# Optimization experiments

Hardware: AMD Instinct MI355X
Metric: run time of the kernel (lower is better)

Reference implementation:

```python
import jax, jax.numpy as jnp
import numpy as np

B, N, FEAT = 64, 1024, 3
HID, STATE, LAYERS, NTYPES = 64, 32, 2, 10


def setup_inputs() -> dict:
    key = jax.random.key(0)
    ks = jax.random.split(key, 16)
    s = 0.1
    return {
        "task_features": jax.random.normal(ks[0], (B, N, FEAT), jnp.float32),
        "task_types": jax.random.randint(ks[1], (B, N), 0, NTYPES, jnp.int32),
        "prev_state": jnp.zeros((B, STATE), jnp.float32),
        "enc_w1": jax.random.normal(ks[2], (HID, FEAT), jnp.float32) * s,
        "enc_b1": jnp.zeros((HID,), jnp.float32),
        "enc_w2": jax.random.normal(ks[3], (HID, HID), jnp.float32) * s,
        "enc_b2": jnp.zeros((HID,), jnp.float32),
        "contention": jax.random.normal(ks[4], (NTYPES, NTYPES), jnp.float32) * 0.1,
        "gnn_w": jax.random.normal(ks[5], (LAYERS, HID, HID), jnp.float32) * s,
        "gnn_b": jnp.zeros((LAYERS, HID), jnp.float32),
        "gru_w_ih": jax.random.normal(ks[6], (3 * STATE, HID), jnp.float32) * s,
        "gru_w_hh": jax.random.normal(ks[7], (3 * STATE, STATE), jnp.float32) * s,
        "gru_b_ih": jnp.zeros((3 * STATE,), jnp.float32),
        "gru_b_hh": jnp.zeros((3 * STATE,), jnp.float32),
        "head_w1": jax.random.normal(ks[8], (HID, HID + STATE), jnp.float32) * s,
        "head_b1": jnp.zeros((HID,), jnp.float32),
        "head_w2": jax.random.normal(ks[9], (1, HID), jnp.float32) * s,
        "head_b2": jnp.zeros((1,), jnp.float32),
    }


def _forward(task_features, task_types, prev_state, enc_w1, enc_b1, enc_w2, enc_b2,
             contention, gnn_w, gnn_b, gru_w_ih, gru_w_hh, gru_b_ih, gru_b_hh,
             head_w1, head_b1, head_w2, head_b2):
    # task encoder: Linear -> ReLU -> Linear
    emb = jax.nn.relu(task_features @ enc_w1.T + enc_b1) @ enc_w2.T + enc_b2  # (B,N,H)
    # interaction graph: type-pair gather + cosine similarity
    base = contention[task_types[:, :, None], task_types[:, None, :]]  # (B,N,N)
    nrm = emb / jnp.maximum(jnp.linalg.norm(emb, axis=-1, keepdims=True), 1e-12)
    sim = jnp.einsum("bnd,bmd->bnm", nrm, nrm)
    adjacency = jax.nn.sigmoid(base) * sim  # (B,N,N)
    # GNN layers: aggregate + linear + relu
    h = emb
    for l in range(LAYERS):
        agg = jnp.einsum("bnm,bmd->bnd", adjacency, h)
        h = jax.nn.relu((h + agg) @ gnn_w[l].T + gnn_b[l])
    ctx = h.mean(axis=1)  # (B,H)
    # GRUCell (torch semantics)
    gi = ctx @ gru_w_ih.T + gru_b_ih
    gh = prev_state @ gru_w_hh.T + gru_b_hh
    i_r, i_z, i_n = jnp.split(gi, 3, axis=-1)
    h_r, h_z, h_n = jnp.split(gh, 3, axis=-1)
    r = jax.nn.sigmoid(i_r + h_r)
    z = jax.nn.sigmoid(i_z + h_z)
    n = jnp.tanh(i_n + r * h_n)
    new_state = (1.0 - z) * n + z * prev_state  # (B,S)
    # latency head on [h, state]
    st = jnp.broadcast_to(new_state[:, None, :], (h.shape[0], h.shape[1], new_state.shape[-1]))
    combined = jnp.concatenate([h, st], axis=-1)
    lat = jax.nn.relu(combined @ head_w1.T + head_b1) @ head_w2.T + head_b2
    return lat[..., 0], new_state


def reference(task_features, task_types, prev_state, enc_w1, enc_b1, enc_w2, enc_b2,
              contention, gnn_w, gnn_b, gru_w_ih, gru_w_hh, gru_b_ih, gru_b_hh,
              head_w1, head_b1, head_w2, head_b2):
    return _forward(task_features, task_types, prev_state, enc_w1, enc_b1, enc_w2, enc_b2,
                    contention, gnn_w, gnn_b, gru_w_ih, gru_w_hh, gru_b_ih, gru_b_hh,
                    head_w1, head_b1, head_w2, head_b2)
```

## Files before the change

kernel.cpp:

```cpp
#include <hip/hip_runtime.h>
#include <math.h>

#define BB 64
#define NN 1024
#define HID 64
#define STATE 32
#define NTYPES 10

typedef _Float16 f16;
typedef f16 f16x8 __attribute__((ext_vector_type(8)));
typedef f16 f16x4 __attribute__((ext_vector_type(4)));
typedef float f32x4 __attribute__((ext_vector_type(4)));

#define MFMA16(a, b, c) __builtin_amdgcn_mfma_f32_16x16x32_f16(a, b, c, 0, 0, 0)

__device__ __forceinline__ float sigm(float x) { return 1.f / (1.f + expf(-x)); }

__device__ __forceinline__ f16x8 cvt8(float4 a, float4 b) {
    f16x8 r;
    r[0] = (f16)a.x; r[1] = (f16)a.y; r[2] = (f16)a.z; r[3] = (f16)a.w;
    r[4] = (f16)b.x; r[5] = (f16)b.y; r[6] = (f16)b.z; r[7] = (f16)b.w;
    return r;
}
__device__ __forceinline__ unsigned packh2(f16 a, f16 b) {
    union { f16 h[2]; unsigned u; } p;
    p.h[0] = a; p.h[1] = b;
    return p.u;
}

__global__ __launch_bounds__(256) void k_misc(
    const float* __restrict__ w2, const float* __restrict__ gw,
    const float* __restrict__ hw1, f16* __restrict__ out,
    int* __restrict__ cnt, float* __restrict__ ctx)
{
    int p = blockIdx.x * 256 + threadIdx.x;
    if (p < 18432) {
        const float* W; int K, pl;
        if (p < 12288) { int seg = p >> 12; pl = p & 4095; W = (seg == 0) ? w2 : gw + (seg - 1) * 4096; K = 64; }
        else { W = hw1; K = 96; pl = p - 12288; }
        int j = pl & 7, lane = (pl >> 3) & 63, nt = (pl >> 9) & 3, ch = pl >> 11;
        int k = ch * 32 + ((lane >> 4) << 3) + j;
        int o = nt * 16 + (lane & 15);
        out[p] = (f16)W[o * K + k];
        return;
    }
    int q = p - 18432;
    if (q < BB * NTYPES) { cnt[q] = 0; return; }
    q -= BB * NTYPES;
    if (q < BB * HID) ctx[q] = 0.f;
}

__global__ __launch_bounds__(256) void k_encoder(
    const float* __restrict__ feat,
    const float* __restrict__ w1, const float* __restrict__ b1,
    const f16* __restrict__ w2f, const float* __restrict__ b2,
    const int* __restrict__ types, int* __restrict__ idx, int* __restrict__ cnt,
    f16* __restrict__ nrm, float* __restrict__ sclv)
{
    __shared__ f16 w2s[4096];
    __shared__ f16 tmp[4][16 * 72];
    __shared__ float fbuf[4][48];
    int tid = threadIdx.x, wave = tid >> 6, lane = tid & 63;
    int l15 = lane & 15, quad = lane >> 4;
    if (tid < 64) {
        int row = blockIdx.x * 64 + tid;
        int b = row >> 10;
        int t = types[row];
        int pos = atomicAdd(&cnt[b * NTYPES + t], 1);
        idx[(b * NTYPES + t) * NN + pos] = row & (NN - 1);
    }
    { const uint4* s = (const uint4*)w2f; uint4* d = (uint4*)w2s;
      for (int i = tid; i < 512; i += 256) d[i] = s[i]; }
    float w10 = w1[lane * 3], w11 = w1[lane * 3 + 1], w12 = w1[lane * 3 + 2], b1l = b1[lane];
    int tb = blockIdx.x * 64 + wave * 16;
    if (lane < 48) fbuf[wave][lane] = feat[tb * 3 + lane];
    __syncthreads();
    f16* tw = &tmp[wave][0];
#pragma unroll
    for (int r = 0; r < 16; ++r) {
        float x0 = fbuf[wave][r * 3], x1 = fbuf[wave][r * 3 + 1], x2 = fbuf[wave][r * 3 + 2];
        float hv = fmaxf(fmaf(w10, x0, fmaf(w11, x1, fmaf(w12, x2, b1l))), 0.f);
        tw[r * 72 + lane] = (f16)hv;
    }
    __builtin_amdgcn_sched_barrier(0);
    f16x8 a0 = *(const f16x8*)&tw[l15 * 72 + quad * 8];
    f16x8 a1 = *(const f16x8*)&tw[l15 * 72 + 32 + quad * 8];
    const f16x8* bf = (const f16x8*)w2s;
    f32x4 acc[4];
#pragma unroll
    for (int nt = 0; nt < 4; ++nt) {
        f32x4 c = {0.f, 0.f, 0.f, 0.f};
        c = MFMA16(a0, bf[(0 * 4 + nt) * 64 + lane], c);
        c = MFMA16(a1, bf[(1 * 4 + nt) * 64 + lane], c);
        acc[nt] = c;
    }
    float b2c[4];
#pragma unroll
    for (int nt = 0; nt < 4; ++nt) b2c[nt] = b2[nt * 16 + l15];
#pragma unroll
    for (int i = 0; i < 4; ++i) {
        float v[4]; float ss = 0.f;
#pragma unroll
        for (int nt = 0; nt < 4; ++nt) { v[nt] = acc[nt][i] + b2c[nt]; ss = fmaf(v[nt], v[nt], ss); }
        ss += __shfl_xor(ss, 1, 64); ss += __shfl_xor(ss, 2, 64);
        ss += __shfl_xor(ss, 4, 64); ss += __shfl_xor(ss, 8, 64);
        float nm = fmaxf(sqrtf(ss), 1e-12f);
        float rinv = 1.f / nm;
        int grow = tb + quad * 4 + i;
#pragma unroll
        for (int nt = 0; nt < 4; ++nt)
            nrm[(size_t)grow * 64 + nt * 16 + l15] = (f16)(v[nt] * rinv);
        if (l15 == 0) sclv[grow] = nm;
    }
}

#define TSTR2 72
__global__ __launch_bounds__(256) void k_buildM(
    const int* __restrict__ idx, const int* __restrict__ cnt,
    const f16* __restrict__ nrm, const f16* __restrict__ h,
    const float* __restrict__ scale, f16* __restrict__ M)
{
    __shared__ f16 nT[64 * TSTR2];
    __shared__ f16 hT[64 * TSTR2];
    int bj = blockIdx.x;
    int b = bj / NTYPES;
    int c = cnt[bj];
    const int* lst = idx + (size_t)bj * NN;
    int tid = threadIdx.x, wave = tid >> 6, lane = tid & 63;
    int l15 = lane & 15, quad = lane >> 4;
    int r = tid & 15;
    int q4 = tid >> 4;
    const f16* nb = nrm + (size_t)b * NN * 64;
    const f16* hb = h + (size_t)b * NN * 64;
    const float* sb = scale ? scale + (size_t)b * NN : nullptr;
    f32x4 acc[4] = {{0.f,0.f,0.f,0.f},{0.f,0.f,0.f,0.f},{0.f,0.f,0.f,0.f},{0.f,0.f,0.f,0.f}};
    for (int k0 = 0; k0 < c; k0 += 64) {
        __syncthreads();
        f16x4 a[4], g[4];
#pragma unroll
        for (int u = 0; u < 4; ++u) { a[u] = (f16x4){0,0,0,0}; g[u] = (f16x4){0,0,0,0}; }
#pragma unroll
        for (int u = 0; u < 4; ++u) {
            int mi = k0 + 4 * r + u;
            if (mi < c) {
                int m = lst[mi];
                a[u] = *(const f16x4*)&nb[(size_t)m * 64 + 4 * q4];
                if (sb) { f16 sm = (f16)sb[m]; f16x4 sv = {sm, sm, sm, sm}; g[u] = a[u] * sv; }
                else g[u] = *(const f16x4*)&hb[(size_t)m * 64 + 4 * q4];
            }
        }
#pragma unroll
        for (int i = 0; i < 4; ++i) {
            *(unsigned*)&nT[(4 * q4 + i) * TSTR2 + 4 * r]     = packh2(a[0][i], a[1][i]);
            *(unsigned*)&nT[(4 * q4 + i) * TSTR2 + 4 * r + 2] = packh2(a[2][i], a[3][i]);
            *(unsigned*)&hT[(4 * q4 + i) * TSTR2 + 4 * r]     = packh2(g[0][i], g[1][i]);
            *(unsigned*)&hT[(4 * q4 + i) * TSTR2 + 4 * r + 2] = packh2(g[2][i], g[3][i]);
        }
        __syncthreads();
        f16x8 af0 = *(const f16x8*)&nT[(wave * 16 + l15) * TSTR2 + quad * 8];
        f16x8 af1 = *(const f16x8*)&nT[(wave * 16 + l15) * TSTR2 + 32 + quad * 8];
#pragma unroll
        for (int nt = 0; nt < 4; ++nt) {
            f16x8 bf0 = *(const f16x8*)&hT[(nt * 16 + l15) * TSTR2 + quad * 8];
            f16x8 bf1 = *(const f16x8*)&hT[(nt * 16 + l15) * TSTR2 + 32 + quad * 8];
            acc[nt] = MFMA16(af0, bf0, acc[nt]);
            acc[nt] = MFMA16(af1, bf1, acc[nt]);
        }
    }
    f16* Mo = M + (size_t)bj * 4096;
#pragma unroll
    for (int nt = 0; nt < 4; ++nt)
#pragma unroll
        for (int i = 0; i < 4; ++i)
            Mo[(wave * 16 + quad * 4 + i) * 64 + nt * 16 + l15] = (f16)acc[nt][i];
}

__global__ __launch_bounds__(256) void k_gnn0_fused(
    const int* __restrict__ idx, const int* __restrict__ cnt,
    const float* __restrict__ cont, const f16* __restrict__ M,
    const f16* __restrict__ nrm, const float* __restrict__ scale,
    const f16* __restrict__ gwf, const float* __restrict__ gb,
    f16* __restrict__ hout, f16* __restrict__ Mout)
{
    __shared__ f16 ds_[4096];
    __shared__ f16 gs[4096];
    __shared__ __align__(16) f16 nT[64 * TSTR2];
    __shared__ __align__(16) f16 hT[64 * TSTR2];
    int i0 = blockIdx.x;
    int xcd = i0 & 7, k = i0 >> 3;
    int b = xcd + 8 * (k / NTYPES);
    int t = k % NTYPES;
    int bt = b * NTYPES + t;
    int c = cnt[bt];
    int tid = threadIdx.x, wave = tid >> 6, lane = tid & 63;
    int l15 = lane & 15, quad = lane >> 4;
    { const uint4* s2 = (const uint4*)gwf; uint4* d2 = (uint4*)gs;
      for (int i = tid; i < 512; i += 256) d2[i] = s2[i]; }
    float sg[NTYPES];
#pragma unroll
    for (int j = 0; j < NTYPES; ++j) sg[j] = sigm(cont[t * NTYPES + j]);
    float ca[16];
#pragma unroll
    for (int i = 0; i < 16; ++i) ca[i] = 0.f;
    const f16* Mb = M + (size_t)b * NTYPES * 4096;
#pragma unroll
    for (int j = 0; j < NTYPES; ++j) {
        const f16* Mr = Mb + j * 4096 + (wave * 16 + l15) * 64;
        f16x8 m0 = *(const f16x8*)&Mr[quad * 8];
        f16x8 m1 = *(const f16x8*)&Mr[32 + quad * 8];
        float sv = sg[j];
#pragma unroll
        for (int e = 0; e < 8; ++e) {
            ca[e]     = fmaf(sv, (float)m0[e], ca[e]);
            ca[8 + e] = fmaf(sv, (float)m1[e], ca[8 + e]);
        }
    }
    f16x8 ca0, ca1;
#pragma unroll
    for (int i = 0; i < 8; ++i) { ca0[i] = (f16)ca[i]; ca1[i] = (f16)ca[8 + i]; }
    __syncthreads();
    const f16x8* gbf = (const f16x8*)gs;
#pragma unroll
    for (int nt = 0; nt < 4; ++nt) {
        f32x4 dd = {0.f, 0.f, 0.f, 0.f};
        dd = MFMA16(ca0, gbf[(0 * 4 + nt) * 64 + lane], dd);
        dd = MFMA16(ca1, gbf[(1 * 4 + nt) * 64 + lane], dd);
#pragma unroll
        for (int i = 0; i < 4; ++i) {
            int d = wave * 16 + quad * 4 + i;
            int pos = (((d >> 5) * 4 + nt) * 64 + ((d >> 3) & 3) * 16 + l15) * 8 + (d & 7);
            ds_[pos] = (f16)dd[i];
        }
    }
    __syncthreads();
    float gbl[4];
#pragma unroll
    for (int nt = 0; nt < 4; ++nt) gbl[nt] = gb[nt * 16 + l15];
    const int* lst = idx + (size_t)bt * NN;
    const f16* nb = nrm + (size_t)b * NN * 64;
    const float* sb = scale + (size_t)b * NN;
    f16* hob = hout + (size_t)b * NN * 64;
    const f16x8* dbf = (const f16x8*)ds_;
    f32x4 macc[4];
#pragma unroll
    for (int nt = 0; nt < 4; ++nt) macc[nt] = (f32x4){0.f, 0.f, 0.f, 0.f};
    int nchunk = (c + 63) >> 6;
    for (int ch = 0; ch < nchunk; ++ch) {
        int tb = ch * 64 + wave * 16;
        int rA = tb + l15;
        bool okA = rA < c;
        int mA = lst[okA ? rA : (c - 1)];
        const f16* na = nb + (size_t)mA * 64;
        f16x8 a0 = *(const f16x8*)&na[quad * 8];
        f16x8 a1 = *(const f16x8*)&na[32 + quad * 8];
        f32x4 acc1[4], acc2[4];
#pragma unroll
        for (int nt = 0; nt < 4; ++nt) {
            f32x4 c1 = {0.f, 0.f, 0.f, 0.f}, c2 = {0.f, 0.f, 0.f, 0.f};
            c1 = MFMA16(a0, dbf[(0 * 4 + nt) * 64 + lane], c1);
            c1 = MFMA16(a1, dbf[(1 * 4 + nt) * 64 + lane], c1);
            c2 = MFMA16(a0, gbf[(0 * 4 + nt) * 64 + lane], c2);
            c2 = MFMA16(a1, gbf[(1 * 4 + nt) * 64 + lane], c2);
            acc1[nt] = c1; acc2[nt] = c2;
        }
        f16x4 hv[4];
#pragma unroll
        for (int nt = 0; nt < 4; ++nt) hv[nt] = (f16x4){0, 0, 0, 0};
#pragma unroll
        for (int i = 0; i < 4; ++i) {
            int rr = tb + quad * 4 + i;
            if (rr < c) {
                int m = lst[rr];
                float sm = sb[m];
#pragma unroll
                for (int nt = 0; nt < 4; ++nt) {
                    float v = fmaxf(fmaf(sm, acc2[nt][i], acc1[nt][i]) + gbl[nt], 0.f);
                    f16 vh = (f16)v;
                    hob[(size_t)m * 64 + nt * 16 + l15] = vh;
                    hv[nt][i] = vh;
                }
            }
        }
        f16x8 z8 = {0, 0, 0, 0, 0, 0, 0, 0};
        f16x8 s0 = okA ? a0 : z8;
        f16x8 s1 = okA ? a1 : z8;
#pragma unroll
        for (int j = 0; j < 8; ++j) {
            nT[(quad * 8 + j) * TSTR2 + wave * 16 + l15]      = s0[j];
            nT[(32 + quad * 8 + j) * TSTR2 + wave * 16 + l15] = s1[j];
        }
#pragma unroll
        for (int nt = 0; nt < 4; ++nt)
            *(f16x4*)&hT[(nt * 16 + l15) * TSTR2 + wave * 16 + quad * 4] = hv[nt];
        __syncthreads();
        f16x8 af0 = *(const f16x8*)&nT[(wave * 16 + l15) * TSTR2 + quad * 8];
        f16x8 af1 = *(const f16x8*)&nT[(wave * 16 + l15) * TSTR2 + 32 + quad * 8];
#pragma unroll
        for (int nt = 0; nt < 4; ++nt) {
            f16x8 bf0 = *(const f16x8*)&hT[(nt * 16 + l15) * TSTR2 + quad * 8];
            f16x8 bf1 = *(const f16x8*)&hT[(nt * 16 + l15) * TSTR2 + 32 + quad * 8];
            macc[nt] = MFMA16(af0, bf0, macc[nt]);
            macc[nt] = MFMA16(af1, bf1, macc[nt]);
        }
        __syncthreads();
    }
    f16* Mo = Mout + (size_t)bt * 4096;
#pragma unroll
    for (int nt = 0; nt < 4; ++nt)
#pragma unroll
        for (int i = 0; i < 4; ++i)
            Mo[(wave * 16 + quad * 4 + i) * 64 + nt * 16 + l15] = (f16)macc[nt][i];
}

__global__ __launch_bounds__(256) void k_gnn_layer(
    const int* __restrict__ idx, const int* __restrict__ cnt,
    const float* __restrict__ cont, const f16* __restrict__ M,
    const f16* __restrict__ nrm, const f16* __restrict__ h,
    const float* __restrict__ scale,
    const f16* __restrict__ gwf, const float* __restrict__ gb,
    f16* __restrict__ hout, float* __restrict__ ctx)
{
    __shared__ f16 ds_[4096];
    __shared__ f16 gs[4096];
    int i0 = blockIdx.x;
    int xcd = i0 & 7, k = i0 >> 3;
    int b = xcd + 8 * (k / NTYPES);
    int t = k % NTYPES;
    int bt = b * NTYPES + t;
    int c = cnt[bt];
    if (c == 0) return;
    int tid = threadIdx.x, wave = tid >> 6, lane = tid & 63;
    int l15 = lane & 15, quad = lane >> 4;
    { const uint4* s2 = (const uint4*)gwf; uint4* d2 = (uint4*)gs;
      for (int i = tid; i < 512; i += 256) d2[i] = s2[i]; }
    float sg[NTYPES];
#pragma unroll
    for (int j = 0; j < NTYPES; ++j) sg[j] = sigm(cont[t * NTYPES + j]);
    float ca[16];
#pragma unroll
    for (int i = 0; i < 16; ++i) ca[i] = 0.f;
    const f16* Mb = M + (size_t)b * NTYPES * 4096;
#pragma unroll
    for (int j = 0; j < NTYPES; ++j) {
        const f16* Mr = Mb + j * 4096 + (wave * 16 + l15) * 64;
        f16x8 m0 = *(const f16x8*)&Mr[quad * 8];
        f16x8 m1 = *(const f16x8*)&Mr[32 + quad * 8];
        float sv = sg[j];
#pragma unroll
        for (int e = 0; e < 8; ++e) {
            ca[e]     = fmaf(sv, (float)m0[e], ca[e]);
            ca[8 + e] = fmaf(sv, (float)m1[e], ca[8 + e]);
        }
    }
    f16x8 ca0, ca1;
#pragma unroll
    for (int i = 0; i < 8; ++i) { ca0[i] = (f16)ca[i]; ca1[i] = (f16)ca[8 + i]; }
    __syncthreads();
    const f16x8* gbf = (const f16x8*)gs;
#pragma unroll
    for (int nt = 0; nt < 4; ++nt) {
        f32x4 dd = {0.f, 0.f, 0.f, 0.f};
        dd = MFMA16(ca0, gbf[(0 * 4 + nt) * 64 + lane], dd);
        dd = MFMA16(ca1, gbf[(1 * 4 + nt) * 64 + lane], dd);
#pragma unroll
        for (int i = 0; i < 4; ++i) {
            int d = wave * 16 + quad * 4 + i;
            int pos = (((d >> 5) * 4 + nt) * 64 + ((d >> 3) & 3) * 16 + l15) * 8 + (d & 7);
            ds_[pos] = (f16)dd[i];
        }
    }
    __syncthreads();
    float gbl[4];
#pragma unroll
    for (int nt = 0; nt < 4; ++nt) gbl[nt] = gb[nt * 16 + l15];
    const int* lst = idx + (size_t)bt * NN;
    const f16* nb = nrm + (size_t)b * NN * 64;
    const f16* hb = h + (size_t)b * NN * 64;
    f16* hob = hout + (size_t)b * NN * 64;
    const f16x8* dbf = (const f16x8*)ds_;
    float cacc[4] = {0.f, 0.f, 0.f, 0.f};
    for (int g = wave; g * 16 < c; g += 4) {
        int tb = g * 16;
        int rA = tb + l15; if (rA >= c) rA = c - 1;
        int mA = lst[rA];
        const f16* na = nb + (size_t)mA * 64;
        f16x8 a0 = *(const f16x8*)&na[quad * 8];
        f16x8 a1 = *(const f16x8*)&na[32 + quad * 8];
        const f16* ha = hb + (size_t)mA * 64;
        f16x8 h0 = *(const f16x8*)&ha[quad * 8];
        f16x8 h1 = *(const f16x8*)&ha[32 + quad * 8];
        f32x4 acc[4];
#pragma unroll
        for (int nt = 0; nt < 4; ++nt) {
            f32x4 cc = {0.f, 0.f, 0.f, 0.f};
            cc = MFMA16(a0, dbf[(0 * 4 + nt) * 64 + lane], cc);
            cc = MFMA16(a1, dbf[(1 * 4 + nt) * 64 + lane], cc);
            cc = MFMA16(h0, gbf[(0 * 4 + nt) * 64 + lane], cc);
            cc = MFMA16(h1, gbf[(1 * 4 + nt) * 64 + lane], cc);
            acc[nt] = cc;
        }
#pragma unroll
        for (int i = 0; i < 4; ++i) {
            int rr = tb + quad * 4 + i;
            if (rr < c) {
                int m = lst[rr];
#pragma unroll
                for (int nt = 0; nt < 4; ++nt) {
                    float v = fmaxf(acc[nt][i] + gbl[nt], 0.f);
                    hob[(size_t)m * 64 + nt * 16 + l15] = (f16)v;
                    cacc[nt] += v;
                }
            }
        }
    }
    if (ctx) {
#pragma unroll
        for (int nt = 0; nt < 4; ++nt) {
            float sv = cacc[nt];
            sv += __shfl_xor(sv, 16, 64);
            sv += __shfl_xor(sv, 32, 64);
            if (quad == 0) atomicAdd(&ctx[b * HID + nt * 16 + l15], sv);
        }
    }
}

__global__ __launch_bounds__(256) void k_head(
    const f16* __restrict__ h2, const float* __restrict__ ctx_sum,
    const float* __restrict__ prev,
    const float* __restrict__ w_ih, const float* __restrict__ w_hh,
    const float* __restrict__ b_ih, const float* __restrict__ b_hh,
    const f16* __restrict__ hwf, const float* __restrict__ b1,
    const float* __restrict__ w2, const float* __restrict__ b2,
    float* __restrict__ lat, float* __restrict__ state_out)
{
    __shared__ f16 ws_[6144];
    __shared__ __align__(16) float st[STATE];
    __shared__ float cs[HID], ps[STATE], gis[96], ghs[96];
    int tid = threadIdx.x, wave = tid >> 6, lane = tid & 63;
    int l15 = lane & 15, quad = lane >> 4;
    int b = blockIdx.x >> 4;
    { const uint4* s = (const uint4*)hwf; uint4* d = (uint4*)ws_;
      for (int i = tid; i < 768; i += 256) d[i] = s[i]; }
    if (tid < HID) cs[tid] = ctx_sum[b * HID + tid] * (1.f / NN);
    if (tid >= HID && tid < HID + STATE) ps[tid - HID] = prev[b * STATE + tid - HID];
    __syncthreads();
    if (tid < 96) {
        float gi = b_ih[tid];
#pragma unroll 8
        for (int k = 0; k < HID; ++k) gi = fmaf(w_ih[tid * HID + k], cs[k], gi);
        float gh = b_hh[tid];
#pragma unroll
        for (int k = 0; k < STATE; ++k) gh = fmaf(w_hh[tid * STATE + k], ps[k], gh);
        gis[tid] = gi; ghs[tid] = gh;
    }
    __syncthreads();
    if (tid < STATE) {
        float r = sigm(gis[tid] + ghs[tid]);
        float z = sigm(gis[32 + tid] + ghs[32 + tid]);
        float nn = tanhf(gis[64 + tid] + r * ghs[64 + tid]);
        float v = (1.f - z) * nn + z * ps[tid];
        st[tid] = v;
        if ((blockIdx.x & 15) == 0) state_out[b * STATE + tid] = v;
    }
    __syncthreads();
    float b1c[4], w2c[4];
#pragma unroll
    for (int nt = 0; nt < 4; ++nt) { b1c[nt] = b1[nt * 16 + l15]; w2c[nt] = w2[nt * 16 + l15]; }
    float b2v = b2[0];
    int tb = blockIdx.x * 64 + wave * 16;
    int grow = tb + l15;
    const f16* ha = h2 + (size_t)grow * 64;
    f16x8 a0 = *(const f16x8*)&ha[quad * 8];
    f16x8 a1 = *(const f16x8*)&ha[32 + quad * 8];
    const float4* sp = (const float4*)st;
    f16x8 a2 = cvt8(sp[quad * 2], sp[quad * 2 + 1]);
    const f16x8* bf = (const f16x8*)ws_;
    f32x4 acc[4];
#pragma unroll
    for (int nt = 0; nt < 4; ++nt) {
        f32x4 cc = {0.f, 0.f, 0.f, 0.f};
        cc = MFMA16(a0, bf[(0 * 4 + nt) * 64 + lane], cc);
        cc = MFMA16(a1, bf[(1 * 4 + nt) * 64 + lane], cc);
        cc = MFMA16(a2, bf[(2 * 4 + nt) * 64 + lane], cc);
        acc[nt] = cc;
    }
#pragma unroll
    for (int i = 0; i < 4; ++i) {
        float s = 0.f;
#pragma unroll
        for (int nt = 0; nt < 4; ++nt) s = fmaf(fmaxf(acc[nt][i] + b1c[nt], 0.f), w2c[nt], s);
        s += __shfl_xor(s, 1, 64); s += __shfl_xor(s, 2, 64);
        s += __shfl_xor(s, 4, 64); s += __shfl_xor(s, 8, 64);
        if (l15 == 0) lat[tb + quad * 4 + i] = s + b2v;
    }
}

extern "C" void kernel_launch(void* const* d_in, const int* in_sizes, int n_in,
                              void* d_out, int out_size, void* d_ws, size_t ws_size,
                              hipStream_t stream) {
    const float* feat   = (const float*)d_in[0];
    const int*   types  = (const int*)d_in[1];
    const float* prev   = (const float*)d_in[2];
    const float* enc_w1 = (const float*)d_in[3];
    const float* enc_b1 = (const float*)d_in[4];
    const float* enc_w2 = (const float*)d_in[5];
    const float* enc_b2 = (const float*)d_in[6];
    const float* cont   = (const float*)d_in[7];
    const float* gnn_w  = (const float*)d_in[8];
    const float* gnn_b  = (const float*)d_in[9];
    const float* w_ih   = (const float*)d_in[10];
    const float* w_hh   = (const float*)d_in[11];
    const float* b_ih   = (const float*)d_in[12];
    const float* b_hh   = (const float*)d_in[13];
    const float* hw1    = (const float*)d_in[14];
    const float* hb1    = (const float*)d_in[15];
    const float* hw2    = (const float*)d_in[16];
    const float* hb2    = (const float*)d_in[17];
    float* out = (float*)d_out;

    float* ws  = (float*)d_ws;
    f16*   nrm = (f16*)ws;
    f16*   h1  = (f16*)(ws + 2097152);
    f16*   h2  = (f16*)(ws + 4194304);
    float* scl = ws + 6291456;
    int*   idx = (int*)(ws + 6356992);
    int*   cnt = idx + BB * NTYPES * NN;
    f16*   M0  = (f16*)(ws + 7012992);
    f16*   M1  = (f16*)(ws + 8323712);
    f16*   wfrag = (f16*)(ws + 9634432);
    float* ctx   = ws + 9643648;
    f16*   w2f  = wfrag;
    f16*   gw0f = wfrag + 4096;
    f16*   gw1f = wfrag + 8192;
    f16*   hwf  = wfrag + 12288;

    k_misc<<<91, 256, 0, stream>>>(enc_w2, gnn_w, hw1, wfrag, cnt, ctx);
    k_encoder<<<BB * NN / 64, 256, 0, stream>>>(feat, enc_w1, enc_b1, w2f, enc_b2,
                                                types, idx, cnt, nrm, scl);
    k_buildM<<<BB * NTYPES, 256, 0, stream>>>(idx, cnt, nrm, nrm, scl, M0);
    k_gnn0_fused<<<BB * NTYPES, 256, 0, stream>>>(idx, cnt, cont, M0, nrm, scl,
                                                  gw0f, gnn_b, h1, M1);
    k_gnn_layer<<<BB * NTYPES, 256, 0, stream>>>(idx, cnt, cont, M1, nrm, h1, nullptr,
                                                 gw1f, gnn_b + HID, h2, ctx);
    k_head<<<BB * NN / 64, 256, 0, stream>>>(h2, ctx, prev, w_ih, w_hh, b_ih, b_hh,
                                             hwf, hb1, hw2, hb2, out, out + BB * NN);
}
```

Baseline: 169.1 us.

## Fuse six pipeline kernels into one cooperative persistent kernel with grid syncs

Replaces the six separate launches (weight packing, encoder, buildM, two GNN layers, head) with a single cooperative kernel of 640 blocks that separates the stages with grid-wide syncs. The aim is to remove per-launch overhead and inter-kernel gaps. Blocks are mapped to batch/type pairs in an XCD-aware order, and the encoder and head stages loop over tiles with a stride of 640. In exchange, every stage is limited to 640 resident blocks and pays a grid barrier, and the GRU is recomputed for every head tile. If the cooperative launch fails, it falls back to the old launches.

```diff
diff --git a/kernel.cpp b/kernel.cpp
--- a/kernel.cpp
+++ b/kernel.cpp
@@ -1,5 +1,8 @@
 #include <hip/hip_runtime.h>
+#include <hip/hip_cooperative_groups.h>
 #include <math.h>
+
+namespace cg = cooperative_groups;
 
 #define BB 64
 #define NN 1024
@@ -27,6 +30,464 @@
     p.h[0] = a; p.h[1] = b;
     return p.u;
 }
+
+struct Args {
+    const float* feat; const int* types; const float* prev;
+    const float* enc_w1; const float* enc_b1; const float* enc_b2;
+    const float* cont; const float* gnn_b;
+    const float* w_ih; const float* w_hh; const float* b_ih; const float* b_hh;
+    const float* hb1; const float* hw2; const float* hb2;
+    const float* enc_w2; const float* gnn_w; const float* hw1;
+    f16* nrm; f16* h1; f16* h2; float* scl; int* idx; int* cnt;
+    f16* M0; f16* M1; f16* wfrag; float* ctx;
+    float* lat; float* state_out;
+};
+
+#define TSTR2 72
+
+__global__ __launch_bounds__(256, 3) void k_mega(Args A)
+{
+    cg::grid_group grid = cg::this_grid();
+    __shared__ __align__(16) unsigned char smem[34816];
+    const int tid = threadIdx.x, wave = tid >> 6, lane = tid & 63;
+    const int l15 = lane & 15, quad = lane >> 4;
+    const int bid = blockIdx.x;
+
+    {
+        int p = bid * 256 + tid;
+        if (p < 18432) {
+            const float* W; int K, pl;
+            if (p < 12288) { int seg = p >> 12; pl = p & 4095;
+                W = (seg == 0) ? A.enc_w2 : A.gnn_w + (seg - 1) * 4096; K = 64; }
+            else { W = A.hw1; K = 96; pl = p - 12288; }
+            int j = pl & 7, ln = (pl >> 3) & 63, nt = (pl >> 9) & 3, ch = pl >> 11;
+            int k = ch * 32 + ((ln >> 4) << 3) + j;
+            int o = nt * 16 + (ln & 15);
+            A.wfrag[p] = (f16)W[o * K + k];
+        } else if (p < 18432 + BB * NTYPES) {
+            A.cnt[p - 18432] = 0;
+        } else if (p < 18432 + BB * NTYPES + BB * HID) {
+            A.ctx[p - 18432 - BB * NTYPES] = 0.f;
+        }
+    }
+    grid.sync();
+
+    {
+        f16* w2s  = (f16*)smem;
+        f16* tmp  = (f16*)(smem + 8192);
+        float* fb = (float*)(smem + 17408);
+        { const uint4* s = (const uint4*)A.wfrag; uint4* d = (uint4*)w2s;
+          for (int i = tid; i < 512; i += 256) d[i] = s[i]; }
+        float w10 = A.enc_w1[lane * 3], w11 = A.enc_w1[lane * 3 + 1],
+              w12 = A.enc_w1[lane * 3 + 2], b1l = A.enc_b1[lane];
+        float b2c[4];
+#pragma unroll
+        for (int nt = 0; nt < 4; ++nt) b2c[nt] = A.enc_b2[nt * 16 + l15];
+        __syncthreads();
+        f16* tw = &tmp[wave * (16 * 72)];
+        float* fw = &fb[wave * 48];
+        const f16x8* bf = (const f16x8*)w2s;
+        for (int tile = bid; tile < BB * NN / 64; tile += 640) {
+            if (tid < 64) {
+                int row = tile * 64 + tid;
+                int b = row >> 10;
+                int t = A.types[row];
+                int pos = atomicAdd(&A.cnt[b * NTYPES + t], 1);
+                A.idx[(b * NTYPES + t) * NN + pos] = row & (NN - 1);
+            }
+            int tb = tile * 64 + wave * 16;
+            if (lane < 48) fw[lane] = A.feat[tb * 3 + lane];
+            __builtin_amdgcn_sched_barrier(0);
+#pragma unroll
+            for (int r = 0; r < 16; ++r) {
+                float x0 = fw[r * 3], x1 = fw[r * 3 + 1], x2 = fw[r * 3 + 2];
+                float hv = fmaxf(fmaf(w10, x0, fmaf(w11, x1, fmaf(w12, x2, b1l))), 0.f);
+                tw[r * 72 + lane] = (f16)hv;
+            }
+            __builtin_amdgcn_sched_barrier(0);
+            f16x8 a0 = *(const f16x8*)&tw[l15 * 72 + quad * 8];
+            f16x8 a1 = *(const f16x8*)&tw[l15 * 72 + 32 + quad * 8];
+            f32x4 acc[4];
+#pragma unroll
+            for (int nt = 0; nt < 4; ++nt) {
+                f32x4 c = {0.f, 0.f, 0.f, 0.f};
+                c = MFMA16(a0, bf[(0 * 4 + nt) * 64 + lane], c);
+                c = MFMA16(a1, bf[(1 * 4 + nt) * 64 + lane], c);
+                acc[nt] = c;
+            }
+#pragma unroll
+            for (int i = 0; i < 4; ++i) {
+                float v[4]; float ss = 0.f;
+#pragma unroll
+                for (int nt = 0; nt < 4; ++nt) { v[nt] = acc[nt][i] + b2c[nt]; ss = fmaf(v[nt], v[nt], ss); }
+                ss += __shfl_xor(ss, 1, 64); ss += __shfl_xor(ss, 2, 64);
+                ss += __shfl_xor(ss, 4, 64); ss += __shfl_xor(ss, 8, 64);
+                float nm = fmaxf(sqrtf(ss), 1e-12f);
+                float rinv = 1.f / nm;
+                int grow = tb + quad * 4 + i;
+#pragma unroll
+                for (int nt = 0; nt < 4; ++nt)
+                    A.nrm[(size_t)grow * 64 + nt * 16 + l15] = (f16)(v[nt] * rinv);
+                if (l15 == 0) A.scl[grow] = nm;
+            }
+        }
+    }
+    grid.sync();
+
+    {
+        f16* nT = (f16*)smem;
+        f16* hT = (f16*)(smem + 9216);
+        int xcd = bid & 7, kk = bid >> 3;
+        int b = xcd + 8 * (kk / NTYPES);
+        int t = kk % NTYPES;
+        int bt = b * NTYPES + t;
+        int c = A.cnt[bt];
+        const int* lst = A.idx + (size_t)bt * NN;
+        int r = tid & 15, q4 = tid >> 4;
+        const f16* nb = A.nrm + (size_t)b * NN * 64;
+        const float* sb = A.scl + (size_t)b * NN;
+        f32x4 acc[4] = {{0.f,0.f,0.f,0.f},{0.f,0.f,0.f,0.f},{0.f,0.f,0.f,0.f},{0.f,0.f,0.f,0.f}};
+        for (int k0 = 0; k0 < c; k0 += 64) {
+            __syncthreads();
+            f16x4 a[4], g[4];
+#pragma unroll
+            for (int u = 0; u < 4; ++u) { a[u] = (f16x4){0,0,0,0}; g[u] = (f16x4){0,0,0,0}; }
+#pragma unroll
+            for (int u = 0; u < 4; ++u) {
+                int mi = k0 + 4 * r + u;
+                if (mi < c) {
+                    int m = lst[mi];
+                    a[u] = *(const f16x4*)&nb[(size_t)m * 64 + 4 * q4];
+                    f16 sm = (f16)sb[m]; f16x4 sv = {sm, sm, sm, sm};
+                    g[u] = a[u] * sv;
+                }
+            }
+#pragma unroll
+            for (int i = 0; i < 4; ++i) {
+                *(unsigned*)&nT[(4 * q4 + i) * TSTR2 + 4 * r]     = packh2(a[0][i], a[1][i]);
+                *(unsigned*)&nT[(4 * q4 + i) * TSTR2 + 4 * r + 2] = packh2(a[2][i], a[3][i]);
+                *(unsigned*)&hT[(4 * q4 + i) * TSTR2 + 4 * r]     = packh2(g[0][i], g[1][i]);
+                *(unsigned*)&hT[(4 * q4 + i) * TSTR2 + 4 * r + 2] = packh2(g[2][i], g[3][i]);
+            }
+            __syncthreads();
+            f16x8 af0 = *(const f16x8*)&nT[(wave * 16 + l15) * TSTR2 + quad * 8];
+            f16x8 af1 = *(const f16x8*)&nT[(wave * 16 + l15) * TSTR2 + 32 + quad * 8];
+#pragma unroll
+            for (int nt = 0; nt < 4; ++nt) {
+                f16x8 bf0 = *(const f16x8*)&hT[(nt * 16 + l15) * TSTR2 + quad * 8];
+                f16x8 bf1 = *(const f16x8*)&hT[(nt * 16 + l15) * TSTR2 + 32 + quad * 8];
+                acc[nt] = MFMA16(af0, bf0, acc[nt]);
+                acc[nt] = MFMA16(af1, bf1, acc[nt]);
+            }
+        }
+        f16* Mo = A.M0 + (size_t)bt * 4096;
+#pragma unroll
+        for (int nt = 0; nt < 4; ++nt)
+#pragma unroll
+            for (int i = 0; i < 4; ++i)
+                Mo[(wave * 16 + quad * 4 + i) * 64 + nt * 16 + l15] = (f16)acc[nt][i];
+    }
+    grid.sync();
+
+    {
+        f16* ds_ = (f16*)smem;
+        f16* gs  = (f16*)(smem + 8192);
+        f16* nT  = (f16*)(smem + 16384);
+        f16* hT  = (f16*)(smem + 25600);
+        int xcd = bid & 7, kk = bid >> 3;
+        int b = xcd + 8 * (kk / NTYPES);
+        int t = kk % NTYPES;
+        int bt = b * NTYPES + t;
+        int c = A.cnt[bt];
+        { const uint4* s2 = (const uint4*)(A.wfrag + 4096); uint4* d2 = (uint4*)gs;
+          for (int i = tid; i < 512; i += 256) d2[i] = s2[i]; }
+        float sg[NTYPES];
+#pragma unroll
+        for (int j = 0; j < NTYPES; ++j) sg[j] = sigm(A.cont[t * NTYPES + j]);
+        float ca[16];
+#pragma unroll
+        for (int i = 0; i < 16; ++i) ca[i] = 0.f;
+        const f16* Mb = A.M0 + (size_t)b * NTYPES * 4096;
+#pragma unroll
+        for (int j = 0; j < NTYPES; ++j) {
+            const f16* Mr = Mb + j * 4096 + (wave * 16 + l15) * 64;
+            f16x8 m0 = *(const f16x8*)&Mr[quad * 8];
+            f16x8 m1 = *(const f16x8*)&Mr[32 + quad * 8];
+            float sv = sg[j];
+#pragma unroll
+            for (int e = 0; e < 8; ++e) {
+                ca[e]     = fmaf(sv, (float)m0[e], ca[e]);
+                ca[8 + e] = fmaf(sv, (float)m1[e], ca[8 + e]);
+            }
+        }
+        f16x8 ca0, ca1;
+#pragma unroll
+        for (int i = 0; i < 8; ++i) { ca0[i] = (f16)ca[i]; ca1[i] = (f16)ca[8 + i]; }
+        __syncthreads();
+        const f16x8* gbf = (const f16x8*)gs;
+#pragma unroll
+        for (int nt = 0; nt < 4; ++nt) {
+            f32x4 dd = {0.f, 0.f, 0.f, 0.f};
+            dd = MFMA16(ca0, gbf[(0 * 4 + nt) * 64 + lane], dd);
+            dd = MFMA16(ca1, gbf[(1 * 4 + nt) * 64 + lane], dd);
+#pragma unroll
+            for (int i = 0; i < 4; ++i) {
+                int d = wave * 16 + quad * 4 + i;
+                int pos = (((d >> 5) * 4 + nt) * 64 + ((d >> 3) & 3) * 16 + l15) * 8 + (d & 7);
+                ds_[pos] = (f16)dd[i];
+            }
+        }
+        __syncthreads();
+        float gbl[4];
+#pragma unroll
+        for (int nt = 0; nt < 4; ++nt) gbl[nt] = A.gnn_b[nt * 16 + l15];
+        const int* lst = A.idx + (size_t)bt * NN;
+        const f16* nb = A.nrm + (size_t)b * NN * 64;
+        const float* sb = A.scl + (size_t)b * NN;
+        f16* hob = A.h1 + (size_t)b * NN * 64;
+        const f16x8* dbf = (const f16x8*)ds_;
+        f32x4 macc[4];
+#pragma unroll
+        for (int nt = 0; nt < 4; ++nt) macc[nt] = (f32x4){0.f, 0.f, 0.f, 0.f};
+        int nchunk = (c + 63) >> 6;
+        for (int ch = 0; ch < nchunk; ++ch) {
+            int tb = ch * 64 + wave * 16;
+            int rA = tb + l15;
+            bool okA = rA < c;
+            int mA = lst[okA ? rA : (c - 1)];
+            const f16* na = nb + (size_t)mA * 64;
+            f16x8 a0 = *(const f16x8*)&na[quad * 8];
+            f16x8 a1 = *(const f16x8*)&na[32 + quad * 8];
+            f32x4 acc1[4], acc2[4];
+#pragma unroll
+            for (int nt = 0; nt < 4; ++nt) {
+                f32x4 c1 = {0.f, 0.f, 0.f, 0.f}, c2 = {0.f, 0.f, 0.f, 0.f};
+                c1 = MFMA16(a0, dbf[(0 * 4 + nt) * 64 + lane], c1);
+                c1 = MFMA16(a1, dbf[(1 * 4 + nt) * 64 + lane], c1);
+                c2 = MFMA16(a0, gbf[(0 * 4 + nt) * 64 + lane], c2);
+                c2 = MFMA16(a1, gbf[(1 * 4 + nt) * 64 + lane], c2);
+                acc1[nt] = c1; acc2[nt] = c2;
+            }
+            f16x4 hv[4];
+#pragma unroll
+            for (int nt = 0; nt < 4; ++nt) hv[nt] = (f16x4){0, 0, 0, 0};
+#pragma unroll
+            for (int i = 0; i < 4; ++i) {
+                int rr = tb + quad * 4 + i;
+                if (rr < c) {
+                    int m = lst[rr];
+                    float sm = sb[m];
+#pragma unroll
+                    for (int nt = 0; nt < 4; ++nt) {
+                        float v = fmaxf(fmaf(sm, acc2[nt][i], acc1[nt][i]) + gbl[nt], 0.f);
+                        f16 vh = (f16)v;
+                        hob[(size_t)m * 64 + nt * 16 + l15] = vh;
+                        hv[nt][i] = vh;
+                    }
+                }
+            }
+            f16x8 z8 = {0, 0, 0, 0, 0, 0, 0, 0};
+            f16x8 s0 = okA ? a0 : z8;
+            f16x8 s1 = okA ? a1 : z8;
+#pragma unroll
+            for (int j = 0; j < 8; ++j) {
+                nT[(quad * 8 + j) * TSTR2 + wave * 16 + l15]      = s0[j];
+                nT[(32 + quad * 8 + j) * TSTR2 + wave * 16 + l15] = s1[j];
+            }
+#pragma unroll
+            for (int nt = 0; nt < 4; ++nt)
+                *(f16x4*)&hT[(nt * 16 + l15) * TSTR2 + wave * 16 + quad * 4] = hv[nt];
+            __syncthreads();
+            f16x8 af0 = *(const f16x8*)&nT[(wave * 16 + l15) * TSTR2 + quad * 8];
+            f16x8 af1 = *(const f16x8*)&nT[(wave * 16 + l15) * TSTR2 + 32 + quad * 8];
+#pragma unroll
+            for (int nt = 0; nt < 4; ++nt) {
+                f16x8 bf0 = *(const f16x8*)&hT[(nt * 16 + l15) * TSTR2 + quad * 8];
+                f16x8 bf1 = *(const f16x8*)&hT[(nt * 16 + l15) * TSTR2 + 32 + quad * 8];
+                macc[nt] = MFMA16(af0, bf0, macc[nt]);
+                macc[nt] = MFMA16(af1, bf1, macc[nt]);
+            }
+            __syncthreads();
+        }
+        f16* Mo = A.M1 + (size_t)bt * 4096;
+#pragma unroll
+        for (int nt = 0; nt < 4; ++nt)
+#pragma unroll
+            for (int i = 0; i < 4; ++i)
+                Mo[(wave * 16 + quad * 4 + i) * 64 + nt * 16 + l15] = (f16)macc[nt][i];
+    }
+    grid.sync();
+
+    {
+        f16* ds_ = (f16*)smem;
+        f16* gs  = (f16*)(smem + 8192);
+        int xcd = bid & 7, kk = bid >> 3;
+        int b = xcd + 8 * (kk / NTYPES);
+        int t = kk % NTYPES;
+        int bt = b * NTYPES + t;
+        int c = A.cnt[bt];
+        if (c != 0) {
+            { const uint4* s2 = (const uint4*)(A.wfrag + 8192); uint4* d2 = (uint4*)gs;
+              for (int i = tid; i < 512; i += 256) d2[i] = s2[i]; }
+            float sg[NTYPES];
+#pragma unroll
+            for (int j = 0; j < NTYPES; ++j) sg[j] = sigm(A.cont[t * NTYPES + j]);
+            float ca[16];
+#pragma unroll
+            for (int i = 0; i < 16; ++i) ca[i] = 0.f;
+            const f16* Mb = A.M1 + (size_t)b * NTYPES * 4096;
+#pragma unroll
+            for (int j = 0; j < NTYPES; ++j) {
+                const f16* Mr = Mb + j * 4096 + (wave * 16 + l15) * 64;
+                f16x8 m0 = *(const f16x8*)&Mr[quad * 8];
+                f16x8 m1 = *(const f16x8*)&Mr[32 + quad * 8];
+                float sv = sg[j];
+#pragma unroll
+                for (int e = 0; e < 8; ++e) {
+                    ca[e]     = fmaf(sv, (float)m0[e], ca[e]);
+                    ca[8 + e] = fmaf(sv, (float)m1[e], ca[8 + e]);
+                }
+            }
+            f16x8 ca0, ca1;
+#pragma unroll
+            for (int i = 0; i < 8; ++i) { ca0[i] = (f16)ca[i]; ca1[i] = (f16)ca[8 + i]; }
+            __syncthreads();
+            const f16x8* gbf = (const f16x8*)gs;
+#pragma unroll
+            for (int nt = 0; nt < 4; ++nt) {
+                f32x4 dd = {0.f, 0.f, 0.f, 0.f};
+                dd = MFMA16(ca0, gbf[(0 * 4 + nt) * 64 + lane], dd);
+                dd = MFMA16(ca1, gbf[(1 * 4 + nt) * 64 + lane], dd);
+#pragma unroll
+                for (int i = 0; i < 4; ++i) {
+                    int d = wave * 16 + quad * 4 + i;
+                    int pos = (((d >> 5) * 4 + nt) * 64 + ((d >> 3) & 3) * 16 + l15) * 8 + (d & 7);
+                    ds_[pos] = (f16)dd[i];
+                }
+            }
+            __syncthreads();
+            float gbl[4];
+#pragma unroll
+            for (int nt = 0; nt < 4; ++nt) gbl[nt] = A.gnn_b[HID + nt * 16 + l15];
+            const int* lst = A.idx + (size_t)bt * NN;
+            const f16* nb = A.nrm + (size_t)b * NN * 64;
+            const f16* hb = A.h1 + (size_t)b * NN * 64;
+            f16* hob = A.h2 + (size_t)b * NN * 64;
+            const f16x8* dbf = (const f16x8*)ds_;
+            float cacc[4] = {0.f, 0.f, 0.f, 0.f};
+            for (int g = wave; g * 16 < c; g += 4) {
+                int tb = g * 16;
+                int rA = tb + l15; if (rA >= c) rA = c - 1;
+                int mA = lst[rA];
+                const f16* na = nb + (size_t)mA * 64;
+                f16x8 a0 = *(const f16x8*)&na[quad * 8];
+                f16x8 a1 = *(const f16x8*)&na[32 + quad * 8];
+                const f16* ha = hb + (size_t)mA * 64;
+                f16x8 h0 = *(const f16x8*)&ha[quad * 8];
+                f16x8 h1v = *(const f16x8*)&ha[32 + quad * 8];
+                f32x4 acc[4];
+#pragma unroll
+                for (int nt = 0; nt < 4; ++nt) {
+                    f32x4 cc = {0.f, 0.f, 0.f, 0.f};
+                    cc = MFMA16(a0, dbf[(0 * 4 + nt) * 64 + lane], cc);
+                    cc = MFMA16(a1, dbf[(1 * 4 + nt) * 64 + lane], cc);
+                    cc = MFMA16(h0, gbf[(0 * 4 + nt) * 64 + lane], cc);
+                    cc = MFMA16(h1v, gbf[(1 * 4 + nt) * 64 + lane], cc);
+                    acc[nt] = cc;
+                }
+#pragma unroll
+                for (int i = 0; i < 4; ++i) {
+                    int rr = tb + quad * 4 + i;
+                    if (rr < c) {
+                        int m = lst[rr];
+#pragma unroll
+                        for (int nt = 0; nt < 4; ++nt) {
+                            float v = fmaxf(acc[nt][i] + gbl[nt], 0.f);
+                            hob[(size_t)m * 64 + nt * 16 + l15] = (f16)v;
+                            cacc[nt] += v;
+                        }
+                    }
+                }
+            }
+#pragma unroll
+            for (int nt = 0; nt < 4; ++nt) {
+                float sv = cacc[nt];
+                sv += __shfl_xor(sv, 16, 64);
+                sv += __shfl_xor(sv, 32, 64);
+                if (quad == 0) atomicAdd(&A.ctx[b * HID + nt * 16 + l15], sv);
+            }
+        }
+    }
+    grid.sync();
+
+    {
+        f16* ws_   = (f16*)smem;
+        float* st  = (float*)(smem + 12288);
+        float* cs  = (float*)(smem + 12416);
+        float* ps  = (float*)(smem + 12672);
+        float* gis = (float*)(smem + 12800);
+        float* ghs = (float*)(smem + 13184);
+        { const uint4* s = (const uint4*)(A.wfrag + 12288); uint4* d = (uint4*)ws_;
+          for (int i = tid; i < 768; i += 256) d[i] = s[i]; }
+        float b1c[4], w2c[4];
+#pragma unroll
+        for (int nt = 0; nt < 4; ++nt) { b1c[nt] = A.hb1[nt * 16 + l15]; w2c[nt] = A.hw2[nt * 16 + l15]; }
+        float b2v = A.hb2[0];
+        const f16x8* bf = (const f16x8*)ws_;
+        for (int tile = bid; tile < BB * NN / 64; tile += 640) {
+            int b = tile >> 4;
+            __syncthreads();
+            if (tid < HID) cs[tid] = A.ctx[b * HID + tid] * (1.f / NN);
+            if (tid >= HID && tid < HID + STATE) ps[tid - HID] = A.prev[b * STATE + tid - HID];
+            __syncthreads();
+            if (tid < 96) {
+                float gi = A.b_ih[tid];
+#pragma unroll 8
+                for (int k = 0; k < HID; ++k) gi = fmaf(A.w_ih[tid * HID + k], cs[k], gi);
+                float gh = A.b_hh[tid];
+#pragma unroll
+                for (int k = 0; k < STATE; ++k) gh = fmaf(A.w_hh[tid * STATE + k], ps[k], gh);
+                gis[tid] = gi; ghs[tid] = gh;
+            }
+            __syncthreads();
+            if (tid < STATE) {
+                float r_ = sigm(gis[tid] + ghs[tid]);
+                float z = sigm(gis[32 + tid] + ghs[32 + tid]);
+                float nn2 = tanhf(gis[64 + tid] + r_ * ghs[64 + tid]);
+                float v = (1.f - z) * nn2 + z * ps[tid];
+                st[tid] = v;
+                if ((tile & 15) == 0) A.state_out[b * STATE + tid] = v;
+            }
+            __syncthreads();
+            int tb = tile * 64 + wave * 16;
+            int grow = tb + l15;
+            const f16* ha = A.h2 + (size_t)grow * 64;
+            f16x8 a0 = *(const f16x8*)&ha[quad * 8];
+            f16x8 a1 = *(const f16x8*)&ha[32 + quad * 8];
+            const float4* sp = (const float4*)st;
+            f16x8 a2 = cvt8(sp[quad * 2], sp[quad * 2 + 1]);
+            f32x4 acc[4];
+#pragma unroll
+            for (int nt = 0; nt < 4; ++nt) {
+                f32x4 cc = {0.f, 0.f, 0.f, 0.f};
+                cc = MFMA16(a0, bf[(0 * 4 + nt) * 64 + lane], cc);
+                cc = MFMA16(a1, bf[(1 * 4 + nt) * 64 + lane], cc);
+                cc = MFMA16(a2, bf[(2 * 4 + nt) * 64 + lane], cc);
+                acc[nt] = cc;
+            }
+#pragma unroll
+            for (int i = 0; i < 4; ++i) {
+                float s = 0.f;
+#pragma unroll
+                for (int nt = 0; nt < 4; ++nt) s = fmaf(fmaxf(acc[nt][i] + b1c[nt], 0.f), w2c[nt], s);
+                s += __shfl_xor(s, 1, 64); s += __shfl_xor(s, 2, 64);
+                s += __shfl_xor(s, 4, 64); s += __shfl_xor(s, 8, 64);
+                if (l15 == 0) A.lat[tb + quad * 4 + i] = s + b2v;
+            }
+        }
+    }
+}
+
 
 __global__ __launch_bounds__(256) void k_misc(
     const float* __restrict__ w2, const float* __restrict__ gw,
@@ -114,7 +575,6 @@
     }
 }
 
-#define TSTR2 72
 __global__ __launch_bounds__(256) void k_buildM(
     const int* __restrict__ idx, const int* __restrict__ cnt,
     const f16* __restrict__ nrm, const f16* __restrict__ h,
@@ -534,14 +994,31 @@
     f16*   gw1f = wfrag + 8192;
     f16*   hwf  = wfrag + 12288;
 
-    k_misc<<<91, 256, 0, stream>>>(enc_w2, gnn_w, hw1, wfrag, cnt, ctx);
-    k_encoder<<<BB * NN / 64, 256, 0, stream>>>(feat, enc_w1, enc_b1, w2f, enc_b2,
-                                                types, idx, cnt, nrm, scl);
-    k_buildM<<<BB * NTYPES, 256, 0, stream>>>(idx, cnt, nrm, nrm, scl, M0);
-    k_gnn0_fused<<<BB * NTYPES, 256, 0, stream>>>(idx, cnt, cont, M0, nrm, scl,
-                                                  gw0f, gnn_b, h1, M1);
-    k_gnn_layer<<<BB * NTYPES, 256, 0, stream>>>(idx, cnt, cont, M1, nrm, h1, nullptr,
-                                                 gw1f, gnn_b + HID, h2, ctx);
-    k_head<<<BB * NN / 64, 256, 0, stream>>>(h2, ctx, prev, w_ih, w_hh, b_ih, b_hh,
-                                             hwf, hb1, hw2, hb2, out, out + BB * NN);
+    Args ha;
+    ha.feat = feat; ha.types = types; ha.prev = prev;
+    ha.enc_w1 = enc_w1; ha.enc_b1 = enc_b1; ha.enc_b2 = enc_b2;
+    ha.cont = cont; ha.gnn_b = gnn_b;
+    ha.w_ih = w_ih; ha.w_hh = w_hh; ha.b_ih = b_ih; ha.b_hh = b_hh;
+    ha.hb1 = hb1; ha.hw2 = hw2; ha.hb2 = hb2;
+    ha.enc_w2 = enc_w2; ha.gnn_w = gnn_w; ha.hw1 = hw1;
+    ha.nrm = nrm; ha.h1 = h1; ha.h2 = h2; ha.scl = scl; ha.idx = idx; ha.cnt = cnt;
+    ha.M0 = M0; ha.M1 = M1; ha.wfrag = wfrag; ha.ctx = ctx;
+    ha.lat = out; ha.state_out = out + BB * NN;
+
+    void* kp[] = { &ha };
+    hipError_t e = hipLaunchCooperativeKernel((void*)k_mega, dim3(640), dim3(256),
+                                              kp, 0, stream);
+    if (e != hipSuccess) {
+        (void)hipGetLastError();
+        k_misc<<<91, 256, 0, stream>>>(enc_w2, gnn_w, hw1, wfrag, cnt, ctx);
+        k_encoder<<<BB * NN / 64, 256, 0, stream>>>(feat, enc_w1, enc_b1, w2f, enc_b2,
+                                                    types, idx, cnt, nrm, scl);
+        k_buildM<<<BB * NTYPES, 256, 0, stream>>>(idx, cnt, nrm, nrm, scl, M0);
+        k_gnn0_fused<<<BB * NTYPES, 256, 0, stream>>>(idx, cnt, cont, M0, nrm, scl,
+                                                      gw0f, gnn_b, h1, M1);
+        k_gnn_layer<<<BB * NTYPES, 256, 0, stream>>>(idx, cnt, cont, M1, nrm, h1, nullptr,
+                                                     gw1f, gnn_b + HID, h2, ctx);
+        k_head<<<BB * NN / 64, 256, 0, stream>>>(h2, ctx, prev, w_ih, w_hh, b_ih, b_hh,
+                                                 hwf, hb1, hw2, hb2, out, out + BB * NN);
+    }
 }
```

Measured after the change: 571.4 us. +238.0%, slower.
